# Kernel optimization log

Measured on AMD Instinct MI355X. Metric: run time of the kernel, lower is better.

## Reference

```python
import jax, jax.numpy as jnp
import numpy as np

B, P, CD, RD, H, NR, OD, T = 1024, 22, 256, 64, 512, 12, 2, 100
IN = OD + 2 + CD + RD  # 324: [pos(2), ball(2), context(256), role_embed(64)]


def setup_inputs() -> dict:
    key = jax.random.key(0)
    ks = jax.random.split(key, 20)
    def n(k, shape, s=1.0):
        return jax.random.normal(k, shape, dtype=jnp.float32) * s
    sH = 1.0 / np.sqrt(H)
    sI = 1.0 / np.sqrt(IN)
    return {
        "context": n(ks[0], (B, P, CD)),
        "initial_position": n(ks[1], (B, P, OD)),
        "ball_landing": n(ks[2], (B, 2)),
        "roles": jax.random.randint(ks[3], (B, P), 0, NR, dtype=jnp.int32),
        "max_steps": T,
        "role_table": n(ks[4], (NR, RD), 0.02),
        # LSTM layer 0 (input_dim=IN)
        "W_ih0": n(ks[5], (4 * H, IN), sI),
        "W_hh0": n(ks[6], (4 * H, H), sH),
        "b0": n(ks[7], (4 * H,), sH),  # b_ih + b_hh fused
        # LSTM layer 1 (input_dim=H)
        "W_ih1": n(ks[8], (4 * H, H), sH),
        "W_hh1": n(ks[9], (4 * H, H), sH),
        "b1": n(ks[10], (4 * H,), sH),
        # output MLP: H -> H//2 -> OD
        "W_fc1": n(ks[11], (H // 2, H), sH),
        "b_fc1": n(ks[12], (H // 2,), sH),
        "W_fc2": n(ks[13], (OD, H // 2), 1.0 / np.sqrt(H // 2)),
        "b_fc2": n(ks[14], (OD,), 0.02),
        # initial_pos_encoder: Linear(OD, H)
        "W_init": n(ks[15], (H, OD), 1.0 / np.sqrt(OD)),
        "b_init": n(ks[16], (H,), 0.02),
    }


def _lstm_cell(x, h, c, W_ih, W_hh, b):
    # PyTorch gate order: i, f, g, o
    gates = x @ W_ih.T + h @ W_hh.T + b  # [N, 4H]
    i, f, g, o = jnp.split(gates, 4, axis=-1)
    c_new = jax.nn.sigmoid(f) * c + jax.nn.sigmoid(i) * jnp.tanh(g)
    h_new = jax.nn.sigmoid(o) * jnp.tanh(c_new)
    return h_new, c_new


def reference(context, initial_position, ball_landing, roles, max_steps,
              role_table, W_ih0, W_hh0, b0, W_ih1, W_hh1, b1,
              W_fc1, b_fc1, W_fc2, b_fc2, W_init, b_init):
    batch, num_players, context_dim = context.shape
    N = batch * num_players
    out_dim = initial_position.shape[-1]

    ctx_flat = context.reshape(N, context_dim)
    role_flat = role_table[roles].reshape(N, -1)
    ball_flat = jnp.broadcast_to(ball_landing[:, None, :], (batch, num_players, 2)).reshape(N, 2)
    static = jnp.concatenate([ball_flat, ctx_flat, role_flat], axis=1)  # [N, IN-2]

    pos0 = initial_position.reshape(N, out_dim)
    h0 = pos0 @ W_init.T + b_init  # initial_pos_encoder into layer-0 hidden
    c0 = jnp.zeros_like(h0)
    h1 = jnp.zeros_like(h0)
    c1 = jnp.zeros_like(h0)

    def step(carry, _):
        pos, h0, c0, h1, c1 = carry
        x = jnp.concatenate([pos, static], axis=1)  # [N, IN]
        h0, c0 = _lstm_cell(x, h0, c0, W_ih0, W_hh0, b0)
        h1, c1 = _lstm_cell(h0, h1, c1, W_ih1, W_hh1, b1)
        # output MLP (dropout inactive in eval)
        nxt = jax.nn.relu(h1 @ W_fc1.T + b_fc1) @ W_fc2.T + b_fc2  # [N, OD]
        return (nxt, h0, c0, h1, c1), nxt

    _, preds = jax.lax.scan(step, (pos0, h0, c0, h1, c1), None, length=max_steps)
    # preds: [T, N, OD] -> [batch, num_players, T, OD]
    preds = preds.transpose(1, 0, 2).reshape(batch, num_players, max_steps, out_dim)
    return preds
```

## Files before the change

### kernel.cpp

```cpp
#include <hip/hip_runtime.h>
#include <cstdint>


#define DEVI __device__ __forceinline__

typedef __bf16 bf16x8 __attribute__((ext_vector_type(8)));
typedef float  f32x4  __attribute__((ext_vector_type(4)));
typedef float  f32x2  __attribute__((ext_vector_type(2)));
typedef unsigned short u16x4 __attribute__((ext_vector_type(4)));
typedef unsigned short u16x8 __attribute__((ext_vector_type(8)));

static constexpr int NROWS = 22528;
static constexpr int NROWSP = 22536;
static constexpr int T_STEPS = 100;
static constexpr int NBM = 176;

DEVI unsigned short f2bf(float f) {
  unsigned u = __float_as_uint(f);
  u = u + 0x7FFFu + ((u >> 16) & 1u);
  return (unsigned short)(u >> 16);
}
DEVI float bf2f(unsigned short h) { return __uint_as_float(((unsigned)h) << 16); }

DEVI float fast_sigmoid(float x) {
  float e = __builtin_amdgcn_exp2f(-1.442695041f * x);
  return __builtin_amdgcn_rcpf(1.0f + e);
}
DEVI float fast_tanh(float x) {
  float e = __builtin_amdgcn_exp2f(2.885390082f * x);
  return 1.0f - 2.0f * __builtin_amdgcn_rcpf(e + 1.0f);
}

DEVI void async_copy16(const void* g, void* l) {
  __builtin_amdgcn_global_load_lds(
      (const __attribute__((address_space(1))) void*)g,
      (__attribute__((address_space(3))) void*)l, 16, 0, 0);
}

#define GBAR   asm volatile("s_barrier" ::: "memory")

template <int KITERS, int KSWITCH>
DEVI void gemm_core(const unsigned short* __restrict__ A1, int lda1,
                    const unsigned short* __restrict__ A2, int lda2,
                    const unsigned short* __restrict__ B1, int ldb1,
                    const unsigned short* __restrict__ B2, int ldb2,
                    unsigned short* lds, f32x4 acc[4][4], int tid) {
  const int lane = tid & 63, wid = tid >> 6;
  const int wm = wid & 1, wn = wid >> 1;
  const int c16 = lane & 15, q = lane >> 4;
#pragma unroll
  for (int i = 0; i < 4; ++i)
#pragma unroll
    for (int j = 0; j < 4; ++j) acc[i][j] = f32x4{0.f, 0.f, 0.f, 0.f};
#pragma unroll
  for (int kt = 0; kt < KITERS; ++kt) {
    const bool sec = (kt >= KSWITCH);
    const unsigned short* Ab = sec ? A2 : A1;
    const unsigned short* Bb = sec ? B2 : B1;
    const int lda = sec ? lda2 : lda1;
    const int ldb = sec ? ldb2 : ldb1;
    const int kk = (sec ? (kt - KSWITCH) : kt) * 64;
    __syncthreads();
#pragma unroll
    for (int rd = 0; rd < 4; ++rd) {
      int p = rd * 256 + tid;
      int row = p >> 3, u = p & 7, ch = u ^ (row & 7);
      async_copy16(Ab + row * lda + kk + ch * 8, lds + p * 8);
      async_copy16(Bb + row * ldb + kk + ch * 8, lds + 8192 + p * 8);
    }
    __syncthreads();
#pragma unroll
    for (int s = 0; s < 2; ++s) {
      bf16x8 a[4], b[4];
#pragma unroll
      for (int mf = 0; mf < 4; ++mf) {
        int row = wm * 64 + mf * 16 + c16;
        int slot = row * 8 + ((s * 4 + q) ^ (row & 7));
        a[mf] = *(const bf16x8*)(lds + slot * 8);
      }
#pragma unroll
      for (int nf = 0; nf < 4; ++nf) {
        int row = wn * 64 + nf * 16 + c16;
        int slot = row * 8 + ((s * 4 + q) ^ (row & 7));
        b[nf] = *(const bf16x8*)(lds + 8192 + slot * 8);
      }
#pragma unroll
      for (int mf = 0; mf < 4; ++mf)
#pragma unroll
        for (int nf = 0; nf < 4; ++nf)
          acc[mf][nf] = __builtin_amdgcn_mfma_f32_16x16x32_bf16(a[mf], b[nf], acc[mf][nf], 0, 0, 0);
    }
  }
}

DEVI int orig_row(int j) {
  int tile = j >> 7, rem = j & 127;
  int half = rem >> 6, g = (rem >> 4) & 3, cc = rem & 15;
  return g * 512 + (tile * 32 + half * 16 + cc);
}

__global__ void k_prep_w(const float* __restrict__ Whh0, const float* __restrict__ Wih1,
                         const float* __restrict__ Whh1, const float* __restrict__ Wih0,
                         const float* __restrict__ Wfc1, const float* __restrict__ b0,
                         const float* __restrict__ b1,
                         unsigned short* __restrict__ W0p, unsigned short* __restrict__ Wc1p,
                         unsigned short* __restrict__ Wsp, unsigned short* __restrict__ Wfc1b,
                         float* __restrict__ Wposx, float* __restrict__ Wposy,
                         float* __restrict__ b0p4, float* __restrict__ b1p4) {
  int j = blockIdx.x;
  int k = threadIdx.x;
  int o = orig_row(j);
  W0p[j * 512 + k]         = f2bf(Whh0[o * 512 + k]);
  Wc1p[j * 1024 + k]       = f2bf(Wih1[o * 512 + k]);
  Wc1p[j * 1024 + 512 + k] = f2bf(Whh1[o * 512 + k]);
  if (k < 384) Wsp[j * 384 + k] = (k < 322) ? f2bf(Wih0[o * 324 + 2 + k]) : (unsigned short)0;
  if (k == 0) {
    int g = (j >> 4) & 3;
    int cg = (j >> 7) * 32 + ((j >> 6) & 1) * 16 + (j & 15);
    Wposx[cg * 4 + g] = Wih0[o * 324 + 0];
    Wposy[cg * 4 + g] = Wih0[o * 324 + 1];
    b0p4[cg * 4 + g] = b0[o];
    b1p4[cg * 4 + g] = b1[o];
  }
  if (j < 256) Wfc1b[j * 512 + k] = f2bf(Wfc1[j * 512 + k]);
}

__global__ void k_init_xs(const float* __restrict__ ball, const float* __restrict__ ctx,
                          const int* __restrict__ roles, const float* __restrict__ role_table,
                          unsigned short* __restrict__ Xs) {
  int n = blockIdx.x, col = threadIdx.x;
  int b = n / 22;
  float v;
  if (col < 2)        v = ball[b * 2 + col];
  else if (col < 258) v = ctx[(size_t)n * 256 + col - 2];
  else if (col < 322) v = role_table[roles[n] * 64 + col - 258];
  else                v = 0.f;
  Xs[(size_t)n * 384 + col] = f2bf(v);
}

__global__ void k_init_p(const float* __restrict__ pos0, const float* __restrict__ Winit,
                         const float* __restrict__ binit,
                         unsigned short* __restrict__ h0A, unsigned short* __restrict__ h1A,
                         float* __restrict__ c0, float* __restrict__ c1,
                         float* __restrict__ posb, unsigned short* __restrict__ SP2) {
  int idx = blockIdx.x * 256 + threadIdx.x;
  if (idx >= NROWSP * 512) return;
  int n = idx >> 9, c = idx & 511;
  if (n < NROWS) {
    float px = pos0[n * 2 + 0], py = pos0[n * 2 + 1];
    h0A[(size_t)n * 512 + c] = f2bf(binit[c] + Winit[c * 2 + 0] * px + Winit[c * 2 + 1] * py);
    if (c < 2) posb[n * 2 + c] = pos0[n * 2 + c];
  } else {
    h0A[(size_t)n * 512 + c] = 0;
    if (c < 2) posb[n * 2 + c] = 0.f;
    ((unsigned long long*)SP2)[(size_t)n * 512 + c] = 0ull;
  }
  h1A[(size_t)n * 512 + c] = 0;
  c0[idx] = 0.f;
  c1[idx] = 0.f;
}

__global__ void k_init_state(const float* __restrict__ pos0, const float* __restrict__ Winit,
                             const float* __restrict__ binit, unsigned short* __restrict__ Hcat,
                             float* __restrict__ c0, float* __restrict__ c1,
                             float* __restrict__ posb) {
  int idx = blockIdx.x * 256 + threadIdx.x;
  if (idx >= NROWS * 512) return;
  int n = idx >> 9, c = idx & 511;
  float px = pos0[n * 2 + 0], py = pos0[n * 2 + 1];
  float h0 = binit[c] + Winit[c * 2 + 0] * px + Winit[c * 2 + 1] * py;
  Hcat[(size_t)n * 1024 + c] = f2bf(h0);
  Hcat[(size_t)n * 1024 + 512 + c] = 0;
  c0[idx] = 0.f;
  c1[idx] = 0.f;
  if (c < 2) posb[n * 2 + c] = pos0[n * 2 + c];
}

__global__ __launch_bounds__(256) void k_static(const unsigned short* __restrict__ Xs,
                                                const unsigned short* __restrict__ Wsp,
                                                const float* __restrict__ b0p4,
                                                unsigned short* __restrict__ SP2) {
  __shared__ __align__(16) unsigned short lds[16384];
  int tid = threadIdx.x, bn = blockIdx.x, bm = blockIdx.y;
  f32x4 acc[4][4];
  const unsigned short* Ab = Xs + (size_t)bm * 128 * 384;
  const unsigned short* Bb = Wsp + (size_t)bn * 128 * 384;
  gemm_core<6, 6>(Ab, 384, Ab, 384, Bb, 384, Bb, 384, lds, acc, tid);
  int lane = tid & 63, wid = tid >> 6, wm = wid & 1, wn = wid >> 1;
  int c16 = lane & 15, q = lane >> 4;
  int cg = bn * 32 + wn * 16 + c16;
  f32x4 bb = *(const f32x4*)&b0p4[cg * 4];
#pragma unroll
  for (int mf = 0; mf < 4; ++mf) {
    int row0 = bm * 128 + wm * 64 + mf * 16 + q * 4;
#pragma unroll
    for (int r = 0; r < 4; ++r) {
      u16x4 v;
      v.x = f2bf(acc[mf][0][r] + bb.x);
      v.y = f2bf(acc[mf][1][r] + bb.y);
      v.z = f2bf(acc[mf][2][r] + bb.z);
      v.w = f2bf(acc[mf][3][r] + bb.w);
      ((u16x4*)SP2)[(size_t)(row0 + r) * 512 + cg] = v;
    }
  }
}


DEVI void stageA_p(const unsigned short* As, int rowbase, int coff,
                   unsigned short* dst, int tid) {
#pragma unroll
  for (int rd = 0; rd < 3; ++rd) {
    int p = rd * 512 + tid;
    int row = p >> 4, gp = p & 15;
    async_copy16(As + (size_t)(rowbase + row) * 512 + coff + (gp ^ (row & 7)) * 8,
                 dst + p * 8);
  }
}

DEVI void stageB_p(const char* Bnt, int ldb, int koff, unsigned short* dst, int tid) {
#pragma unroll
  for (int ks = 0; ks < 2; ++ks)
#pragma unroll
    for (int rd = 0; rd < 2; ++rd) {
      int p = rd * 512 + tid;
      int j = p >> 2, u = p & 3, ch = u ^ ((j >> 1) & 3);
      async_copy16(Bnt + (size_t)j * ldb + koff + ks * 64 + ch * 16,
                   dst + ks * 8192 + p * 8);
    }
}

template <int KT, int KSW>
DEVI void gemm_p(const unsigned short* A1, const unsigned short* A2, int rowbase,
                 const char* Bnt, int ldb,
                 unsigned short* Abuf, unsigned short* Bbuf,
                 f32x4 acc[3][4], int tid) {
  const int lane = tid & 63, wid = tid >> 6;
  const int wm = wid >> 2, wn = wid & 3;
  const int c16 = lane & 15, q = lane >> 4;
#pragma unroll
  for (int i = 0; i < 3; ++i)
#pragma unroll
    for (int j = 0; j < 4; ++j) acc[i][j] = f32x4{0.f, 0.f, 0.f, 0.f};
  stageA_p(A1, rowbase, 0, Abuf, tid);
  stageB_p(Bnt, ldb, 0, Bbuf, tid);
#pragma unroll
  for (int kt = 0; kt < KT; ++kt) {
    GBAR;
    int nIss = 0;
    if (kt + 1 < KT) { stageB_p(Bnt, ldb, (kt + 1) * 128, Bbuf + ((kt + 1) & 1) * 16384, tid); nIss += 4; }
    if ((kt & 1) == 0 && (kt / 2 + 1) < KT / 2) {
      int c = kt / 2 + 1;
      const unsigned short* As = (c < KSW / 2) ? A1 : A2;
      int coff = ((c < KSW / 2) ? c : (c - KSW / 2)) * 128;
      stageA_p(As, rowbase, coff, Abuf + (c & 1) * 12288, tid);
      nIss += 3;
    }
    if (nIss == 7)      asm volatile("s_waitcnt vmcnt(7)" ::: "memory");
    else if (nIss == 4) asm volatile("s_waitcnt vmcnt(4)" ::: "memory");
    else if (nIss == 3) asm volatile("s_waitcnt vmcnt(3)" ::: "memory");
    else                asm volatile("s_waitcnt vmcnt(0)" ::: "memory");
    GBAR;
    const unsigned short* Ab = Abuf + ((kt >> 1) & 1) * 12288;
    const unsigned short* Bb = Bbuf + (kt & 1) * 16384;
#pragma unroll
    for (int ks = 0; ks < 2; ++ks) {
      bf16x8 a[3], b[4];
#pragma unroll
      for (int mf = 0; mf < 3; ++mf) {
        int rl = wm * 48 + mf * 16 + c16;
        int g = (kt & 1) * 8 + ks * 4 + q;
        a[mf] = *(const bf16x8*)(Ab + rl * 128 + (g ^ (rl & 7)) * 8);
      }
#pragma unroll
      for (int nf = 0; nf < 4; ++nf) {
        int jl = wn * 64 + nf * 16 + c16;
        b[nf] = *(const bf16x8*)(Bb + ks * 8192 + (jl * 4 + (q ^ ((jl >> 1) & 3))) * 8);
      }
      __builtin_amdgcn_s_setprio(1);
#pragma unroll
      for (int mf = 0; mf < 3; ++mf)
#pragma unroll
        for (int nf = 0; nf < 4; ++nf)
          acc[mf][nf] = __builtin_amdgcn_mfma_f32_16x16x32_bf16(a[mf], b[nf], acc[mf][nf], 0, 0, 0);
      __builtin_amdgcn_s_setprio(0);
    }
    __builtin_amdgcn_sched_barrier(0);
  }
}

__global__ __launch_bounds__(512, 2) void k_persist(
    const unsigned short* __restrict__ W0p, const unsigned short* __restrict__ Wc1p,
    const unsigned short* __restrict__ Wfc1b, const unsigned short* __restrict__ SP2,
    const float* __restrict__ b1p4,
    const float* __restrict__ Wposx, const float* __restrict__ Wposy,
    const float* __restrict__ bfc1, const float* __restrict__ Wfc2,
    const float* __restrict__ bfc2,
    unsigned short* __restrict__ h0A, unsigned short* __restrict__ h0B,
    unsigned short* __restrict__ h1A, unsigned short* __restrict__ h1B,
    float* __restrict__ c0, float* __restrict__ c1,
    float* __restrict__ posb, float* __restrict__ out) {
  __shared__ __align__(16) unsigned short Abuf[2 * 12288];
  __shared__ __align__(16) unsigned short Bbuf[2 * 16384];
  __shared__ float wfc2s[512];
  __shared__ float red[96 * 8];
  const int tid = threadIdx.x, blk = blockIdx.x;
  const int lane = tid & 63, wid = tid >> 6;
  const int wm = wid >> 2, wn = wid & 3;
  const int c16 = lane & 15, q = lane >> 4;
  const int rowbase = blk * 88;
  wfc2s[tid] = Wfc2[tid];
  __syncthreads();
  f32x4 acc[3][4];
#pragma unroll 1
  for (int t = 0; t < T_STEPS; ++t) {
    const unsigned short* h0p = (t & 1) ? h0B : h0A;
    unsigned short*       h0n = (t & 1) ? h0A : h0B;
    const unsigned short* h1p = (t & 1) ? h1B : h1A;
    unsigned short*       h1n = (t & 1) ? h1A : h1B;
#pragma unroll 1
    for (int nt = 0; nt < 8; ++nt) {
      gemm_p<8, 8>(h0p, h0p, rowbase, (const char*)W0p + (size_t)nt * 256 * 1024, 1024,
                   Abuf, Bbuf, acc, tid);
      const int cg = nt * 64 + (wn >> 1) * 32 + (wn & 1) * 16 + c16;
      f32x4 wpx = *(const f32x4*)&Wposx[cg * 4];
      f32x4 wpy = *(const f32x4*)&Wposy[cg * 4];
#pragma unroll
      for (int mf = 0; mf < 3; ++mf) {
        int row0 = rowbase + wm * 48 + mf * 16 + q * 4;
        f32x4 cold = *(const f32x4*)&c0[(size_t)cg * NROWSP + row0];
        f32x4 cnew;
#pragma unroll
        for (int r = 0; r < 4; ++r) {
          size_t row = row0 + r;
          f32x2 pv = *(const f32x2*)&posb[row * 2];
          u16x4 sp = ((const u16x4*)SP2)[row * 512 + cg];
          float gi = acc[mf][0][r] + bf2f(sp.x) + pv.x * wpx.x + pv.y * wpy.x;
          float gf = acc[mf][1][r] + bf2f(sp.y) + pv.x * wpx.y + pv.y * wpy.y;
          float gg = acc[mf][2][r] + bf2f(sp.z) + pv.x * wpx.z + pv.y * wpy.z;
          float go = acc[mf][3][r] + bf2f(sp.w) + pv.x * wpx.w + pv.y * wpy.w;
          float cn = fast_sigmoid(gf) * cold[r] + fast_sigmoid(gi) * fast_tanh(gg);
          cnew[r] = cn;
          h0n[row * 512 + cg] = f2bf(fast_sigmoid(go) * fast_tanh(cn));
        }
        *(f32x4*)&c0[(size_t)cg * NROWSP + row0] = cnew;
      }
      __syncthreads();
    }
#pragma unroll 1
    for (int nt = 0; nt < 8; ++nt) {
      gemm_p<16, 8>(h0n, h1p, rowbase, (const char*)Wc1p + (size_t)nt * 256 * 2048, 2048,
                    Abuf, Bbuf, acc, tid);
      const int cg = nt * 64 + (wn >> 1) * 32 + (wn & 1) * 16 + c16;
      f32x4 bv = *(const f32x4*)&b1p4[cg * 4];
#pragma unroll
      for (int mf = 0; mf < 3; ++mf) {
        int row0 = rowbase + wm * 48 + mf * 16 + q * 4;
        f32x4 cold = *(const f32x4*)&c1[(size_t)cg * NROWSP + row0];
        f32x4 cnew;
#pragma unroll
        for (int r = 0; r < 4; ++r) {
          size_t row = row0 + r;
          float gi = acc[mf][0][r] + bv.x;
          float gf = acc[mf][1][r] + bv.y;
          float gg = acc[mf][2][r] + bv.z;
          float go = acc[mf][3][r] + bv.w;
          float cn = fast_sigmoid(gf) * cold[r] + fast_sigmoid(gi) * fast_tanh(gg);
          cnew[r] = cn;
          h1n[row * 512 + cg] = f2bf(fast_sigmoid(go) * fast_tanh(cn));
        }
        *(f32x4*)&c1[(size_t)cg * NROWSP + row0] = cnew;
      }
      __syncthreads();
    }
    {
      gemm_p<8, 8>(h1n, h1n, rowbase, (const char*)Wfc1b, 1024, Abuf, Bbuf, acc, tid);
      float part[2][3][4];
#pragma unroll
      for (int d = 0; d < 2; ++d)
#pragma unroll
        for (int mf = 0; mf < 3; ++mf)
#pragma unroll
          for (int r = 0; r < 4; ++r) part[d][mf][r] = 0.f;
#pragma unroll
      for (int nf = 0; nf < 4; ++nf) {
        int col = wn * 64 + nf * 16 + c16;
        float w0 = wfc2s[col], w1 = wfc2s[256 + col], bv = bfc1[col];
#pragma unroll
        for (int mf = 0; mf < 3; ++mf)
#pragma unroll
          for (int r = 0; r < 4; ++r) {
            float v = acc[mf][nf][r] + bv;
            v = v > 0.f ? v : 0.f;
            part[0][mf][r] += v * w0;
            part[1][mf][r] += v * w1;
          }
      }
#pragma unroll
      for (int st = 1; st < 16; st <<= 1)
#pragma unroll
        for (int d = 0; d < 2; ++d)
#pragma unroll
          for (int mf = 0; mf < 3; ++mf)
#pragma unroll
            for (int r = 0; r < 4; ++r)
              part[d][mf][r] += __shfl_xor(part[d][mf][r], st, 64);
      if (c16 == 0) {
#pragma unroll
        for (int mf = 0; mf < 3; ++mf)
#pragma unroll
          for (int r = 0; r < 4; ++r) {
            int rl = wm * 48 + mf * 16 + q * 4 + r;
            red[rl * 8 + wn * 2 + 0] = part[0][mf][r];
            red[rl * 8 + wn * 2 + 1] = part[1][mf][r];
          }
      }
      __syncthreads();
      if (tid < 192) {
        int rl = tid >> 1, d = tid & 1;
        float s = red[rl * 8 + d] + red[rl * 8 + 2 + d] + red[rl * 8 + 4 + d]
                + red[rl * 8 + 6 + d] + bfc2[d];
        if (rl < 88) {
          int rg = rowbase + rl;
          out[((size_t)rg * T_STEPS + t) * 2 + d] = s;
          posb[rg * 2 + d] = s;
        }
      }
      __syncthreads();
    }
  }
}

struct GemmSrc {
  const unsigned short *A1, *A2, *B1, *B2;
  int ldA1, ldA2, ldB1, ldB2;
};

template <int KT, int KSW>
DEVI void stage_q(const GemmSrc& g, int t, int s, int isB, unsigned short* dst, int tid) {
  int tt = (t >= KT) ? (t - 2) : t;
  const bool sec = (tt >= KSW);
  const unsigned short* base;
  int ld;
  if (isB) { base = sec ? g.B2 : g.B1; ld = sec ? g.ldB2 : g.ldB1; }
  else     { base = sec ? g.A2 : g.A1; ld = sec ? g.ldA2 : g.ldA1; }
  base += (sec ? (tt - KSW) : tt) * 64 + s * 32;
#pragma unroll
  for (int rd = 0; rd < 2; ++rd) {
    int p = rd * 512 + tid;
    int row = p >> 2, u = p & 3, ch = u ^ ((row >> 1) & 3);
    async_copy16(base + row * ld + ch * 8, dst + p * 8);
  }
}

#define VMCNT4 asm volatile("s_waitcnt vmcnt(4)" ::: "memory")

template <int KT, int KSW>
DEVI void gemm8(const GemmSrc& g, unsigned short* lds, f32x4 acc[8][4], int tid) {
  const int lane = tid & 63, wid = tid >> 6;
  const int wm = wid >> 2, wn = wid & 3;
  const int c16 = lane & 15, q = lane >> 4;
#pragma unroll
  for (int i = 0; i < 8; ++i)
#pragma unroll
    for (int j = 0; j < 4; ++j) acc[i][j] = f32x4{0.f, 0.f, 0.f, 0.f};
  unsigned short* A00 = lds;
  unsigned short* A01 = lds + 8192;
  unsigned short* B00 = lds + 16384;
  unsigned short* B01 = lds + 24576;
  unsigned short* A10 = lds + 32768;
  unsigned short* A11 = lds + 40960;
  unsigned short* B10 = lds + 49152;
  unsigned short* B11 = lds + 57344;
  const int rowA0 = wm * 128 + c16;
  const int rowB0 = wn * 64 + c16;
  stage_q<KT, KSW>(g, 0, 0, 0, A00, tid);
  stage_q<KT, KSW>(g, 0, 0, 1, B00, tid);
  stage_q<KT, KSW>(g, 0, 1, 0, A01, tid);
// ... 15 lines not shown
    int row = rowB0 + f * 16;                                                  \
    b[f] = *(const bf16x8*)((BASE) + (row * 4 + (q ^ ((row >> 1) & 3))) * 8);  \
  }
#define MFG(MG)                                                                \
  __builtin_amdgcn_s_setprio(1);                                               \
  _Pragma("unroll")                                                            \
  for (int f = 0; f < 4; ++f)                                                  \
    _Pragma("unroll")                                                          \
    for (int nf = 0; nf < 4; ++nf)                                             \
      acc[(MG) * 4 + f][nf] = __builtin_amdgcn_mfma_f32_16x16x32_bf16(         \
          a[f], b[nf], acc[(MG) * 4 + f][nf], 0, 0, 0);                        \
  __builtin_amdgcn_s_setprio(0);                                               \
  __builtin_amdgcn_sched_barrier(0);
#pragma unroll 1
  for (int it = 0; it < KT / 2; ++it) {
    const int t0 = 2 * it;
    LOADA(A00, 0); LOADB(B00);
    stage_q<KT, KSW>(g, t0 + 1, 1, 0, A11, tid);
    GBAR; MFG(0); GBAR;
    LOADA(A00, 1);
    stage_q<KT, KSW>(g, t0 + 1, 1, 1, B11, tid);
    GBAR; MFG(1); GBAR;
    LOADA(A01, 0); LOADB(B01);
    stage_q<KT, KSW>(g, t0 + 2, 0, 0, A00, tid);
    GBAR; MFG(0); GBAR;
    LOADA(A01, 1);
    stage_q<KT, KSW>(g, t0 + 2, 0, 1, B00, tid);
    GBAR; MFG(1); VMCNT4; GBAR;
    LOADA(A10, 0); LOADB(B10);
    stage_q<KT, KSW>(g, t0 + 2, 1, 0, A01, tid);
    GBAR; MFG(0); GBAR;
    LOADA(A10, 1);
    stage_q<KT, KSW>(g, t0 + 2, 1, 1, B01, tid);
    GBAR; MFG(1); GBAR;
    LOADA(A11, 0); LOADB(B11);
    stage_q<KT, KSW>(g, t0 + 3, 0, 0, A10, tid);
    GBAR; MFG(0); GBAR;
    LOADA(A11, 1);
    stage_q<KT, KSW>(g, t0 + 3, 0, 1, B10, tid);
    GBAR; MFG(1); VMCNT4; GBAR;
  }
  asm volatile("s_waitcnt vmcnt(0)" ::: "memory");
#undef LOADA
#undef LOADB
#undef MFG
}

DEVI void swz704(int l, int& bn, int& bm) {
  int xcd = l & 7, ii = l >> 3;
  bn = ii & 7;
  bm = (ii >> 3) * 8 + xcd;
}

__global__ __launch_bounds__(512, 2) void k_s1_lite(const unsigned short* __restrict__ cur,
                                                    const unsigned short* __restrict__ Xs,
                                                    const unsigned short* __restrict__ W0p,
                                                    const unsigned short* __restrict__ Wsp,
                                                    const float* __restrict__ b0p4,
                                                    const float* __restrict__ Wposx,
                                                    const float* __restrict__ Wposy,
                                                    const float* __restrict__ posb,
                                                    float* __restrict__ c0,
                                                    unsigned short* __restrict__ nxt) {
  __shared__ __align__(16) unsigned short lds[65536];
  const int tid = threadIdx.x;
  int bn, bm;
  swz704(blockIdx.x, bn, bm);
  f32x4 acc[8][4];
  GemmSrc g;
  g.A1 = cur + (size_t)bm * 256 * 1024; g.ldA1 = 1024;
  g.B1 = W0p + (size_t)bn * 256 * 512;  g.ldB1 = 512;
  g.A2 = Xs + (size_t)bm * 256 * 384;   g.ldA2 = 384;
  g.B2 = Wsp + (size_t)bn * 256 * 384;  g.ldB2 = 384;
  gemm8<14, 8>(g, lds, acc, tid);
  const int lane = tid & 63, wid = tid >> 6;
  const int wm = wid >> 2, wn = wid & 3;
  const int c16 = lane & 15, q = lane >> 4;
  const int cg = bn * 64 + (wn >> 1) * 32 + (wn & 1) * 16 + c16;
  f32x4 wpx = *(const f32x4*)&Wposx[cg * 4];
  f32x4 wpy = *(const f32x4*)&Wposy[cg * 4];
  f32x4 sb = *(const f32x4*)&b0p4[cg * 4];
#pragma unroll
  for (int mf = 0; mf < 8; ++mf) {
    int row0 = bm * 256 + wm * 128 + mf * 16 + q * 4;
    f32x4 cold = *(const f32x4*)&c0[(size_t)cg * NROWS + row0];
    f32x4 cnew;
#pragma unroll
    for (int r = 0; r < 4; ++r) {
      size_t row = row0 + r;
      f32x2 pv = *(const f32x2*)&posb[row * 2];
      float gi = acc[mf][0][r] + sb.x + pv.x * wpx.x + pv.y * wpy.x;
      float gf = acc[mf][1][r] + sb.y + pv.x * wpx.y + pv.y * wpy.y;
      float gg = acc[mf][2][r] + sb.z + pv.x * wpx.z + pv.y * wpy.z;
      float go = acc[mf][3][r] + sb.w + pv.x * wpx.w + pv.y * wpy.w;
      float cn = fast_sigmoid(gf) * cold[r] + fast_sigmoid(gi) * fast_tanh(gg);
      cnew[r] = cn;
      nxt[row * 1024 + cg] = f2bf(fast_sigmoid(go) * fast_tanh(cn));
    }
    *(f32x4*)&c0[(size_t)cg * NROWS + row0] = cnew;
  }
}

__global__ __launch_bounds__(512, 2) void k_s2_8(const unsigned short* __restrict__ nxt_in,
                                                 const unsigned short* __restrict__ cur,
                                                 const unsigned short* __restrict__ Wc1p,
                                                 const float* __restrict__ b1p4,
// ... 131 lines not shown
#pragma unroll
    for (int mf = 0; mf < 2; ++mf)
#pragma unroll
      for (int r = 0; r < 4; ++r) {
        int rl = mf * 16 + q * 4 + r;
        red[rl * 8 + wid * 2 + 0] = part[0][mf][r];
        red[rl * 8 + wid * 2 + 1] = part[1][mf][r];
      }
  }
  __syncthreads();
  if (tid < 64) {
    int rl = tid >> 1, d = tid & 1;
    float s = red[rl * 8 + d] + red[rl * 8 + 2 + d] + red[rl * 8 + 4 + d]
            + red[rl * 8 + 6 + d] + bfc2[d];
    int rg = b32 * 32 + rl;
    out[((size_t)rg * T_STEPS + t) * 2 + d] = s;
    posb[rg * 2 + d] = s;
  }
}

extern "C" void kernel_launch(void* const* d_in, const int* in_sizes, int n_in,
                              void* d_out, int out_size, void* d_ws, size_t ws_size,
                              hipStream_t stream) {
  (void)in_sizes; (void)n_in; (void)out_size;
  const float* ctx   = (const float*)d_in[0];
  const float* pos0  = (const float*)d_in[1];
  const float* ball  = (const float*)d_in[2];
  const int*   roles = (const int*)d_in[3];
  const float* role_table = (const float*)d_in[5];
  const float* Wih0 = (const float*)d_in[6];
  const float* Whh0 = (const float*)d_in[7];
  const float* b0   = (const float*)d_in[8];
  const float* Wih1 = (const float*)d_in[9];
  const float* Whh1 = (const float*)d_in[10];
  const float* b1   = (const float*)d_in[11];
  const float* Wfc1 = (const float*)d_in[12];
  const float* bfc1 = (const float*)d_in[13];
  const float* Wfc2 = (const float*)d_in[14];
  const float* bfc2 = (const float*)d_in[15];
  const float* Winit = (const float*)d_in[16];
  const float* binit = (const float*)d_in[17];
  float* out = (float*)d_out;

  char* w = (char*)d_ws;
  size_t used = 0;
  auto alloc = [&](size_t bytes) {
    char* p = w + used;
    used += (bytes + 255) & ~(size_t)255;
    return p;
  };
  unsigned short* W0p   = (unsigned short*)alloc((size_t)2048 * 512 * 2);
  unsigned short* Wc1p  = (unsigned short*)alloc((size_t)2048 * 1024 * 2);
  unsigned short* Wfc1b = (unsigned short*)alloc((size_t)256 * 512 * 2);
  float* Wposx = (float*)alloc(2048 * 4);
  float* Wposy = (float*)alloc(2048 * 4);
  float* b0p4  = (float*)alloc(2048 * 4);
  float* b1p4  = (float*)alloc(2048 * 4);
  float* posb  = (float*)alloc((size_t)NROWSP * 2 * 4);
  unsigned short* h0A = (unsigned short*)alloc((size_t)NROWSP * 512 * 2);
  unsigned short* h0B = (unsigned short*)alloc((size_t)NROWSP * 512 * 2);
  unsigned short* h1A = (unsigned short*)alloc((size_t)NROWSP * 512 * 2);
  unsigned short* h1B = (unsigned short*)alloc((size_t)NROWSP * 512 * 2);
  float* c0   = (float*)alloc((size_t)512 * NROWSP * 4);
  float* c1   = (float*)alloc((size_t)512 * NROWSP * 4);
  unsigned short* SP2 = (unsigned short*)alloc((size_t)NROWSP * 2048 * 2);
  unsigned short* Xs  = h0B;
  unsigned short* Wsp = h1B;

  const bool use_p = (ws_size >= used + (1u << 20));

  if (use_p) {
    k_prep_w<<<2048, 512, 0, stream>>>(Whh0, Wih1, Whh1, Wih0, Wfc1, b0, b1,
                                       W0p, Wc1p, Wsp, Wfc1b, Wposx, Wposy, b0p4, b1p4);
    k_init_xs<<<NROWS, 384, 0, stream>>>(ball, ctx, roles, role_table, Xs);
    k_init_p<<<(NROWSP * 512 + 255) / 256, 256, 0, stream>>>(pos0, Winit, binit,
                                                             h0A, h1A, c0, c1, posb, SP2);
    dim3 gs(16, NBM);
    k_static<<<gs, 256, 0, stream>>>(Xs, Wsp, b0p4, SP2);
    k_persist<<<256, 512, 0, stream>>>(W0p, Wc1p, Wfc1b, SP2, b1p4, Wposx, Wposy,
                                       bfc1, Wfc2, bfc2, h0A, h0B, h1A, h1B,
                                       c0, c1, posb, out);
  } else {
    used = 0;
    unsigned short* W0pL   = (unsigned short*)alloc((size_t)2048 * 512 * 2);
    unsigned short* Wc1pL  = (unsigned short*)alloc((size_t)2048 * 1024 * 2);
    unsigned short* Wfc1bL = (unsigned short*)alloc((size_t)256 * 512 * 2);
    float* WposxL = (float*)alloc(2048 * 4);
    float* WposyL = (float*)alloc(2048 * 4);
    float* b0p4L  = (float*)alloc(2048 * 4);
    float* b1p4L  = (float*)alloc(2048 * 4);
    float* posbL  = (float*)alloc((size_t)NROWS * 2 * 4);
    unsigned short* Hc0 = (unsigned short*)alloc((size_t)NROWS * 1024 * 2);
    float* c0L   = (float*)alloc((size_t)NROWS * 512 * 4);
    float* c1L   = (float*)alloc((size_t)NROWS * 512 * 4);
    unsigned short* Hc1 = (unsigned short*)alloc((size_t)NROWS * 1024 * 2);
    unsigned short* XsL  = (unsigned short*)alloc((size_t)NROWS * 384 * 2);
    unsigned short* WspL = (unsigned short*)alloc((size_t)2048 * 384 * 2);

    k_prep_w<<<2048, 512, 0, stream>>>(Whh0, Wih1, Whh1, Wih0, Wfc1, b0, b1,
                                       W0pL, Wc1pL, WspL, Wfc1bL, WposxL, WposyL, b0p4L, b1p4L);
    k_init_xs<<<NROWS, 384, 0, stream>>>(ball, ctx, roles, role_table, XsL);
    k_init_state<<<(NROWS * 512 + 255) / 256, 256, 0, stream>>>(pos0, Winit, binit, Hc0,
                                                                c0L, c1L, posbL);
    for (int t = 0; t < T_STEPS; ++t) {
      unsigned short* cur = (t & 1) ? Hc1 : Hc0;
      unsigned short* nxt = (t & 1) ? Hc0 : Hc1;
      k_s1_lite<<<704, 512, 0, stream>>>(cur, XsL, W0pL, WspL, b0p4L,
                                         WposxL, WposyL, posbL, c0L, nxt);
      k_s2_8<<<704, 512, 0, stream>>>(nxt, cur, Wc1pL, b1p4L, c1L, nxt);
      k_s3<<<704, 256, 0, stream>>>(nxt, Wfc1bL, bfc1, Wfc2, bfc2, out, posbL, t);
    }
  }
}
```

Measured before the change: 21.52 ms.

## Fold static input projection into per-step layer-0 GEMM and halve persistent block size

Drops the precomputed static-gate buffer (SP2) and the separate static GEMM kernel. The layer-0 GEMM in the persistent kernel now concatenates h0 with the static inputs Xs along K (28 k-iters of 64 instead of 8 of 128), so the static projection is recomputed every timestep rather than read as a 22536x2048 bf16 buffer. The persistent kernel moves from 256 blocks of 512 threads with 88 rows each to 512 blocks of 256 threads with 44 rows each, with one M-wave per block. This trades a large per-step memory read for extra MFMA work each step and changes the occupancy and tiling, while removing the preprocessing GEMM.

```diff
diff --git a/kernel.cpp b/kernel.cpp
--- a/kernel.cpp
+++ b/kernel.cpp
@@ -8,12 +8,10 @@
 typedef float  f32x4  __attribute__((ext_vector_type(4)));
 typedef float  f32x2  __attribute__((ext_vector_type(2)));
 typedef unsigned short u16x4 __attribute__((ext_vector_type(4)));
-typedef unsigned short u16x8 __attribute__((ext_vector_type(8)));
 
 static constexpr int NROWS = 22528;
 static constexpr int NROWSP = 22536;
 static constexpr int T_STEPS = 100;
-static constexpr int NBM = 176;
 
 DEVI unsigned short f2bf(float f) {
   unsigned u = __float_as_uint(f);
@@ -37,61 +35,7 @@
       (__attribute__((address_space(3))) void*)l, 16, 0, 0);
 }
 
-#define GBAR   asm volatile("s_barrier" ::: "memory")
-
-template <int KITERS, int KSWITCH>
-DEVI void gemm_core(const unsigned short* __restrict__ A1, int lda1,
-                    const unsigned short* __restrict__ A2, int lda2,
-                    const unsigned short* __restrict__ B1, int ldb1,
-                    const unsigned short* __restrict__ B2, int ldb2,
-                    unsigned short* lds, f32x4 acc[4][4], int tid) {
-  const int lane = tid & 63, wid = tid >> 6;
-  const int wm = wid & 1, wn = wid >> 1;
-  const int c16 = lane & 15, q = lane >> 4;
-#pragma unroll
-  for (int i = 0; i < 4; ++i)
-#pragma unroll
-    for (int j = 0; j < 4; ++j) acc[i][j] = f32x4{0.f, 0.f, 0.f, 0.f};
-#pragma unroll
-  for (int kt = 0; kt < KITERS; ++kt) {
-    const bool sec = (kt >= KSWITCH);
-    const unsigned short* Ab = sec ? A2 : A1;
-    const unsigned short* Bb = sec ? B2 : B1;
-    const int lda = sec ? lda2 : lda1;
-    const int ldb = sec ? ldb2 : ldb1;
-    const int kk = (sec ? (kt - KSWITCH) : kt) * 64;
-    __syncthreads();
-#pragma unroll
-    for (int rd = 0; rd < 4; ++rd) {
-      int p = rd * 256 + tid;
-      int row = p >> 3, u = p & 7, ch = u ^ (row & 7);
-      async_copy16(Ab + row * lda + kk + ch * 8, lds + p * 8);
-      async_copy16(Bb + row * ldb + kk + ch * 8, lds + 8192 + p * 8);
-    }
-    __syncthreads();
-#pragma unroll
-    for (int s = 0; s < 2; ++s) {
-      bf16x8 a[4], b[4];
-#pragma unroll
-      for (int mf = 0; mf < 4; ++mf) {
-        int row = wm * 64 + mf * 16 + c16;
-        int slot = row * 8 + ((s * 4 + q) ^ (row & 7));
-        a[mf] = *(const bf16x8*)(lds + slot * 8);
-      }
-#pragma unroll
-      for (int nf = 0; nf < 4; ++nf) {
-        int row = wn * 64 + nf * 16 + c16;
-        int slot = row * 8 + ((s * 4 + q) ^ (row & 7));
-        b[nf] = *(const bf16x8*)(lds + 8192 + slot * 8);
-      }
-#pragma unroll
-      for (int mf = 0; mf < 4; ++mf)
-#pragma unroll
-        for (int nf = 0; nf < 4; ++nf)
-          acc[mf][nf] = __builtin_amdgcn_mfma_f32_16x16x32_bf16(a[mf], b[nf], acc[mf][nf], 0, 0, 0);
-    }
-  }
-}
+#define GBAR asm volatile("s_barrier" ::: "memory")
 
 DEVI int orig_row(int j) {
   int tile = j >> 7, rem = j & 127;
@@ -125,16 +69,17 @@
   if (j < 256) Wfc1b[j * 512 + k] = f2bf(Wfc1[j * 512 + k]);
 }
 
-__global__ void k_init_xs(const float* __restrict__ ball, const float* __restrict__ ctx,
-                          const int* __restrict__ roles, const float* __restrict__ role_table,
-                          unsigned short* __restrict__ Xs) {
+__global__ void k_init_xs_p(const float* __restrict__ ball, const float* __restrict__ ctx,
+                            const int* __restrict__ roles, const float* __restrict__ role_table,
+                            unsigned short* __restrict__ Xs) {
   int n = blockIdx.x, col = threadIdx.x;
-  int b = n / 22;
-  float v;
-  if (col < 2)        v = ball[b * 2 + col];
-  else if (col < 258) v = ctx[(size_t)n * 256 + col - 2];
-  else if (col < 322) v = role_table[roles[n] * 64 + col - 258];
-  else                v = 0.f;
+  float v = 0.f;
+  if (n < NROWS) {
+    int b = n / 22;
+    if (col < 2)        v = ball[b * 2 + col];
+    else if (col < 258) v = ctx[(size_t)n * 256 + col - 2];
+    else if (col < 322) v = role_table[roles[n] * 64 + col - 258];
+  }
   Xs[(size_t)n * 384 + col] = f2bf(v);
 }
 
@@ -142,117 +87,79 @@
                          const float* __restrict__ binit,
                          unsigned short* __restrict__ h0A, unsigned short* __restrict__ h1A,
                          float* __restrict__ c0, float* __restrict__ c1,
-                         float* __restrict__ posb, unsigned short* __restrict__ SP2) {
+                         float* __restrict__ posb) {
   int idx = blockIdx.x * 256 + threadIdx.x;
   if (idx >= NROWSP * 512) return;
   int n = idx >> 9, c = idx & 511;
+  unsigned short h0 = 0;
   if (n < NROWS) {
     float px = pos0[n * 2 + 0], py = pos0[n * 2 + 1];
-    h0A[(size_t)n * 512 + c] = f2bf(binit[c] + Winit[c * 2 + 0] * px + Winit[c * 2 + 1] * py);
+    h0 = f2bf(binit[c] + Winit[c * 2 + 0] * px + Winit[c * 2 + 1] * py);
     if (c < 2) posb[n * 2 + c] = pos0[n * 2 + c];
   } else {
-    h0A[(size_t)n * 512 + c] = 0;
     if (c < 2) posb[n * 2 + c] = 0.f;
-    ((unsigned long long*)SP2)[(size_t)n * 512 + c] = 0ull;
-  }
+  }
+  h0A[(size_t)n * 512 + c] = h0;
   h1A[(size_t)n * 512 + c] = 0;
   c0[idx] = 0.f;
   c1[idx] = 0.f;
 }
 
-__global__ void k_init_state(const float* __restrict__ pos0, const float* __restrict__ Winit,
-                             const float* __restrict__ binit, unsigned short* __restrict__ Hcat,
-                             float* __restrict__ c0, float* __restrict__ c1,
-                             float* __restrict__ posb) {
-  int idx = blockIdx.x * 256 + threadIdx.x;
-  if (idx >= NROWS * 512) return;
-  int n = idx >> 9, c = idx & 511;
-  float px = pos0[n * 2 + 0], py = pos0[n * 2 + 1];
-  float h0 = binit[c] + Winit[c * 2 + 0] * px + Winit[c * 2 + 1] * py;
-  Hcat[(size_t)n * 1024 + c] = f2bf(h0);
-  Hcat[(size_t)n * 1024 + 512 + c] = 0;
-  c0[idx] = 0.f;
-  c1[idx] = 0.f;
-  if (c < 2) posb[n * 2 + c] = pos0[n * 2 + c];
-}
-
-__global__ __launch_bounds__(256) void k_static(const unsigned short* __restrict__ Xs,
-                                                const unsigned short* __restrict__ Wsp,
-                                                const float* __restrict__ b0p4,
-                                                unsigned short* __restrict__ SP2) {
-  __shared__ __align__(16) unsigned short lds[16384];
-  int tid = threadIdx.x, bn = blockIdx.x, bm = blockIdx.y;
-  f32x4 acc[4][4];
-  const unsigned short* Ab = Xs + (size_t)bm * 128 * 384;
-  const unsigned short* Bb = Wsp + (size_t)bn * 128 * 384;
-  gemm_core<6, 6>(Ab, 384, Ab, 384, Bb, 384, Bb, 384, lds, acc, tid);
-  int lane = tid & 63, wid = tid >> 6, wm = wid & 1, wn = wid >> 1;
-  int c16 = lane & 15, q = lane >> 4;
-  int cg = bn * 32 + wn * 16 + c16;
-  f32x4 bb = *(const f32x4*)&b0p4[cg * 4];
-#pragma unroll
-  for (int mf = 0; mf < 4; ++mf) {
-    int row0 = bm * 128 + wm * 64 + mf * 16 + q * 4;
-#pragma unroll
-    for (int r = 0; r < 4; ++r) {
-      u16x4 v;
-      v.x = f2bf(acc[mf][0][r] + bb.x);
-      v.y = f2bf(acc[mf][1][r] + bb.y);
-      v.z = f2bf(acc[mf][2][r] + bb.z);
-      v.w = f2bf(acc[mf][3][r] + bb.w);
-      ((u16x4*)SP2)[(size_t)(row0 + r) * 512 + cg] = v;
-    }
-  }
-}
-
-
-DEVI void stageA_p(const unsigned short* As, int rowbase, int coff,
-                   unsigned short* dst, int tid) {
+
+DEVI void stA2(const unsigned short* As, int lda, int rb, int coff,
+               unsigned short* dst, int tid) {
 #pragma unroll
   for (int rd = 0; rd < 3; ++rd) {
-    int p = rd * 512 + tid;
+    int p = rd * 256 + tid;
     int row = p >> 4, gp = p & 15;
-    async_copy16(As + (size_t)(rowbase + row) * 512 + coff + (gp ^ (row & 7)) * 8,
+    async_copy16(As + (size_t)(rb + row) * lda + coff + (gp ^ (row & 7)) * 8,
                  dst + p * 8);
   }
 }
 
-DEVI void stageB_p(const char* Bnt, int ldb, int koff, unsigned short* dst, int tid) {
-#pragma unroll
-  for (int ks = 0; ks < 2; ++ks)
-#pragma unroll
-    for (int rd = 0; rd < 2; ++rd) {
-      int p = rd * 512 + tid;
-      int j = p >> 2, u = p & 3, ch = u ^ ((j >> 1) & 3);
-      async_copy16(Bnt + (size_t)j * ldb + koff + ks * 64 + ch * 16,
-                   dst + ks * 8192 + p * 8);
-    }
-}
-
-template <int KT, int KSW>
-DEVI void gemm_p(const unsigned short* A1, const unsigned short* A2, int rowbase,
-                 const char* Bnt, int ldb,
-                 unsigned short* Abuf, unsigned short* Bbuf,
-                 f32x4 acc[3][4], int tid) {
-  const int lane = tid & 63, wid = tid >> 6;
-  const int wm = wid >> 2, wn = wid & 3;
+DEVI void stB2(const char* B, int ldb, int koff, unsigned short* dst, int tid) {
+#pragma unroll
+  for (int rd = 0; rd < 4; ++rd) {
+    int p = rd * 256 + tid;
+    int j = p >> 2, u = p & 3, ch = u ^ ((j >> 1) & 3);
+    async_copy16(B + (size_t)j * ldb + koff + ch * 16, dst + p * 8);
+  }
+}
+
+struct Src2 {
+  const unsigned short *A1, *A2; int ldA1, ldA2;
+  const char *B1, *B2; int ldB1, ldB2;
+};
+
+template <int KT, int ASW, int BSW>
+DEVI void gemm2(const Src2& s, int rb, unsigned short* Ab2, unsigned short* Bb2,
+                f32x4 acc[3][4], int tid) {
+  const int lane = tid & 63, wn = tid >> 6;
   const int c16 = lane & 15, q = lane >> 4;
 #pragma unroll
   for (int i = 0; i < 3; ++i)
 #pragma unroll
     for (int j = 0; j < 4; ++j) acc[i][j] = f32x4{0.f, 0.f, 0.f, 0.f};
-  stageA_p(A1, rowbase, 0, Abuf, tid);
-  stageB_p(Bnt, ldb, 0, Bbuf, tid);
+  stA2(s.A1, s.ldA1, rb, 0, Ab2, tid);
+  stB2(s.B1, s.ldB1, 0, Bb2, tid);
 #pragma unroll
   for (int kt = 0; kt < KT; ++kt) {
     GBAR;
     int nIss = 0;
-    if (kt + 1 < KT) { stageB_p(Bnt, ldb, (kt + 1) * 128, Bbuf + ((kt + 1) & 1) * 16384, tid); nIss += 4; }
-    if ((kt & 1) == 0 && (kt / 2 + 1) < KT / 2) {
-      int c = kt / 2 + 1;
-      const unsigned short* As = (c < KSW / 2) ? A1 : A2;
-      int coff = ((c < KSW / 2) ? c : (c - KSW / 2)) * 128;
-      stageA_p(As, rowbase, coff, Abuf + (c & 1) * 12288, tid);
+    if (kt + 1 < KT) {
+      const int kb = kt + 1;
+      const char* Bp = (kb < BSW) ? s.B1 : s.B2;
+      const int ldb = (kb < BSW) ? s.ldB1 : s.ldB2;
+      const int ko = ((kb < BSW) ? kb : (kb - BSW)) * 64;
+      stB2(Bp, ldb, ko, Bb2 + (kb & 1) * 8192, tid);
+      nIss += 4;
+    }
+    if ((kt & 3) == 0 && (kt / 4 + 1) < KT / 4) {
+      const int c = kt / 4 + 1;
+      const unsigned short* Ap = (c < ASW) ? s.A1 : s.A2;
+      const int lda = (c < ASW) ? s.ldA1 : s.ldA2;
+      const int co = ((c < ASW) ? c : (c - ASW)) * 128;
+      stA2(Ap, lda, rb, co, Ab2 + (c & 1) * 6144, tid);
       nIss += 3;
     }
     if (nIss == 7)      asm volatile("s_waitcnt vmcnt(7)" ::: "memory");
@@ -260,38 +167,36 @@
     else if (nIss == 3) asm volatile("s_waitcnt vmcnt(3)" ::: "memory");
     else                asm volatile("s_waitcnt vmcnt(0)" ::: "memory");
     GBAR;
-    const unsigned short* Ab = Abuf + ((kt >> 1) & 1) * 12288;
-    const unsigned short* Bb = Bbuf + (kt & 1) * 16384;
-#pragma unroll
-    for (int ks = 0; ks < 2; ++ks) {
-      bf16x8 a[3], b[4];
-#pragma unroll
-      for (int mf = 0; mf < 3; ++mf) {
-        int rl = wm * 48 + mf * 16 + c16;
-        int g = (kt & 1) * 8 + ks * 4 + q;
-        a[mf] = *(const bf16x8*)(Ab + rl * 128 + (g ^ (rl & 7)) * 8);
-      }
-#pragma unroll
-      for (int nf = 0; nf < 4; ++nf) {
-        int jl = wn * 64 + nf * 16 + c16;
-        b[nf] = *(const bf16x8*)(Bb + ks * 8192 + (jl * 4 + (q ^ ((jl >> 1) & 3))) * 8);
-      }
-      __builtin_amdgcn_s_setprio(1);
-#pragma unroll
-      for (int mf = 0; mf < 3; ++mf)
-#pragma unroll
-        for (int nf = 0; nf < 4; ++nf)
-          acc[mf][nf] = __builtin_amdgcn_mfma_f32_16x16x32_bf16(a[mf], b[nf], acc[mf][nf], 0, 0, 0);
-      __builtin_amdgcn_s_setprio(0);
-    }
+    const unsigned short* Ab = Ab2 + ((kt >> 2) & 1) * 6144;
+    const unsigned short* Bb = Bb2 + (kt & 1) * 8192;
+    bf16x8 a[3], b[4];
+#pragma unroll
+    for (int mf = 0; mf < 3; ++mf) {
+      int rl = mf * 16 + c16;
+      int g = (kt & 3) * 4 + q;
+      a[mf] = *(const bf16x8*)(Ab + (rl * 16 + (g ^ (rl & 7))) * 8);
+    }
+#pragma unroll
+    for (int nf = 0; nf < 4; ++nf) {
+      int jl = wn * 64 + nf * 16 + c16;
+      b[nf] = *(const bf16x8*)(Bb + (jl * 4 + (q ^ ((jl >> 1) & 3))) * 8);
+    }
+    __builtin_amdgcn_s_setprio(1);
+#pragma unroll
+    for (int mf = 0; mf < 3; ++mf)
+#pragma unroll
+      for (int nf = 0; nf < 4; ++nf)
+        acc[mf][nf] = __builtin_amdgcn_mfma_f32_16x16x32_bf16(a[mf], b[nf], acc[mf][nf], 0, 0, 0);
+    __builtin_amdgcn_s_setprio(0);
     __builtin_amdgcn_sched_barrier(0);
   }
 }
 
-__global__ __launch_bounds__(512, 2) void k_persist(
+__global__ __launch_bounds__(256, 2) void k_persist2(
     const unsigned short* __restrict__ W0p, const unsigned short* __restrict__ Wc1p,
-    const unsigned short* __restrict__ Wfc1b, const unsigned short* __restrict__ SP2,
-    const float* __restrict__ b1p4,
+    const unsigned short* __restrict__ Wfc1b, const unsigned short* __restrict__ Wsp,
+    const unsigned short* __restrict__ Xs,
+    const float* __restrict__ b0p4, const float* __restrict__ b1p4,
     const float* __restrict__ Wposx, const float* __restrict__ Wposy,
     const float* __restrict__ bfc1, const float* __restrict__ Wfc2,
     const float* __restrict__ bfc2,
@@ -299,16 +204,16 @@
     unsigned short* __restrict__ h1A, unsigned short* __restrict__ h1B,
     float* __restrict__ c0, float* __restrict__ c1,
     float* __restrict__ posb, float* __restrict__ out) {
-  __shared__ __align__(16) unsigned short Abuf[2 * 12288];
-  __shared__ __align__(16) unsigned short Bbuf[2 * 16384];
+  __shared__ __align__(16) unsigned short Ab2[2 * 6144];
+  __shared__ __align__(16) unsigned short Bb2[2 * 8192];
   __shared__ float wfc2s[512];
-  __shared__ float red[96 * 8];
+  __shared__ float red[48 * 8];
   const int tid = threadIdx.x, blk = blockIdx.x;
-  const int lane = tid & 63, wid = tid >> 6;
-  const int wm = wid >> 2, wn = wid & 3;
+  const int lane = tid & 63, wn = tid >> 6;
   const int c16 = lane & 15, q = lane >> 4;
-  const int rowbase = blk * 88;
+  const int rb = blk * 44;
   wfc2s[tid] = Wfc2[tid];
+  wfc2s[tid + 256] = Wfc2[tid + 256];
   __syncthreads();
   f32x4 acc[3][4];
 #pragma unroll 1
@@ -319,42 +224,50 @@
     unsigned short*       h1n = (t & 1) ? h1A : h1B;
 #pragma unroll 1
     for (int nt = 0; nt < 8; ++nt) {
-      gemm_p<8, 8>(h0p, h0p, rowbase, (const char*)W0p + (size_t)nt * 256 * 1024, 1024,
-                   Abuf, Bbuf, acc, tid);
+      Src2 s;
+      s.A1 = h0p; s.ldA1 = 512; s.A2 = Xs; s.ldA2 = 384;
+      s.B1 = (const char*)W0p + (size_t)nt * 256 * 1024; s.ldB1 = 1024;
+      s.B2 = (const char*)Wsp + (size_t)nt * 256 * 768;  s.ldB2 = 768;
+      gemm2<28, 4, 16>(s, rb, Ab2, Bb2, acc, tid);
       const int cg = nt * 64 + (wn >> 1) * 32 + (wn & 1) * 16 + c16;
       f32x4 wpx = *(const f32x4*)&Wposx[cg * 4];
       f32x4 wpy = *(const f32x4*)&Wposy[cg * 4];
+      f32x4 sb  = *(const f32x4*)&b0p4[cg * 4];
 #pragma unroll
       for (int mf = 0; mf < 3; ++mf) {
-        int row0 = rowbase + wm * 48 + mf * 16 + q * 4;
+        const bool live = !(mf == 2 && q == 3);
+        int row0 = rb + mf * 16 + q * 4;
         f32x4 cold = *(const f32x4*)&c0[(size_t)cg * NROWSP + row0];
         f32x4 cnew;
 #pragma unroll
         for (int r = 0; r < 4; ++r) {
           size_t row = row0 + r;
           f32x2 pv = *(const f32x2*)&posb[row * 2];
-          u16x4 sp = ((const u16x4*)SP2)[row * 512 + cg];
-          float gi = acc[mf][0][r] + bf2f(sp.x) + pv.x * wpx.x + pv.y * wpy.x;
-          float gf = acc[mf][1][r] + bf2f(sp.y) + pv.x * wpx.y + pv.y * wpy.y;
-          float gg = acc[mf][2][r] + bf2f(sp.z) + pv.x * wpx.z + pv.y * wpy.z;
-          float go = acc[mf][3][r] + bf2f(sp.w) + pv.x * wpx.w + pv.y * wpy.w;
+          float gi = acc[mf][0][r] + sb.x + pv.x * wpx.x + pv.y * wpy.x;
+          float gf = acc[mf][1][r] + sb.y + pv.x * wpx.y + pv.y * wpy.y;
+          float gg = acc[mf][2][r] + sb.z + pv.x * wpx.z + pv.y * wpy.z;
+          float go = acc[mf][3][r] + sb.w + pv.x * wpx.w + pv.y * wpy.w;
           float cn = fast_sigmoid(gf) * cold[r] + fast_sigmoid(gi) * fast_tanh(gg);
           cnew[r] = cn;
-          h0n[row * 512 + cg] = f2bf(fast_sigmoid(go) * fast_tanh(cn));
+          if (live) h0n[row * 512 + cg] = f2bf(fast_sigmoid(go) * fast_tanh(cn));
         }
-        *(f32x4*)&c0[(size_t)cg * NROWSP + row0] = cnew;
+        if (live) *(f32x4*)&c0[(size_t)cg * NROWSP + row0] = cnew;
       }
       __syncthreads();
     }
 #pragma unroll 1
     for (int nt = 0; nt < 8; ++nt) {
-      gemm_p<16, 8>(h0n, h1p, rowbase, (const char*)Wc1p + (size_t)nt * 256 * 2048, 2048,
-                    Abuf, Bbuf, acc, tid);
+      Src2 s;
+      s.A1 = h0n; s.ldA1 = 512; s.A2 = h1p; s.ldA2 = 512;
+      s.B1 = (const char*)Wc1p + (size_t)nt * 256 * 2048; s.ldB1 = 2048;
+      s.B2 = s.B1; s.ldB2 = 2048;
+      gemm2<32, 4, 32>(s, rb, Ab2, Bb2, acc, tid);
       const int cg = nt * 64 + (wn >> 1) * 32 + (wn & 1) * 16 + c16;
       f32x4 bv = *(const f32x4*)&b1p4[cg * 4];
 #pragma unroll
       for (int mf = 0; mf < 3; ++mf) {
-        int row0 = rowbase + wm * 48 + mf * 16 + q * 4;
+        const bool live = !(mf == 2 && q == 3);
+        int row0 = rb + mf * 16 + q * 4;
         f32x4 cold = *(const f32x4*)&c1[(size_t)cg * NROWSP + row0];
         f32x4 cnew;
 #pragma unroll
@@ -366,14 +279,18 @@
           float go = acc[mf][3][r] + bv.w;
           float cn = fast_sigmoid(gf) * cold[r] + fast_sigmoid(gi) * fast_tanh(gg);
           cnew[r] = cn;
-          h1n[row * 512 + cg] = f2bf(fast_sigmoid(go) * fast_tanh(cn));
+          if (live) h1n[row * 512 + cg] = f2bf(fast_sigmoid(go) * fast_tanh(cn));
         }
-        *(f32x4*)&c1[(size_t)cg * NROWSP + row0] = cnew;
+        if (live) *(f32x4*)&c1[(size_t)cg * NROWSP + row0] = cnew;
       }
       __syncthreads();
     }
     {
-      gemm_p<8, 8>(h1n, h1n, rowbase, (const char*)Wfc1b, 1024, Abuf, Bbuf, acc, tid);
+      Src2 s;
+      s.A1 = h1n; s.ldA1 = 512; s.A2 = h1n; s.ldA2 = 512;
+      s.B1 = (const char*)Wfc1b; s.ldB1 = 1024;
+      s.B2 = s.B1; s.ldB2 = 1024;
+      gemm2<16, 4, 16>(s, rb, Ab2, Bb2, acc, tid);
       float part[2][3][4];
 #pragma unroll
       for (int d = 0; d < 2; ++d)
@@ -409,20 +326,20 @@
         for (int mf = 0; mf < 3; ++mf)
 #pragma unroll
           for (int r = 0; r < 4; ++r) {
-            int rl = wm * 48 + mf * 16 + q * 4 + r;
+            int rl = mf * 16 + q * 4 + r;
             red[rl * 8 + wn * 2 + 0] = part[0][mf][r];
             red[rl * 8 + wn * 2 + 1] = part[1][mf][r];
           }
       }
       __syncthreads();
-      if (tid < 192) {
+      if (tid < 96) {
         int rl = tid >> 1, d = tid & 1;
-        float s = red[rl * 8 + d] + red[rl * 8 + 2 + d] + red[rl * 8 + 4 + d]
-                + red[rl * 8 + 6 + d] + bfc2[d];
-        if (rl < 88) {
-          int rg = rowbase + rl;
-          out[((size_t)rg * T_STEPS + t) * 2 + d] = s;
-          posb[rg * 2 + d] = s;
+        float sum = red[rl * 8 + d] + red[rl * 8 + 2 + d] + red[rl * 8 + 4 + d]
+                  + red[rl * 8 + 6 + d] + bfc2[d];
+        if (rl < 44) {
+          int rg = rb + rl;
+          out[((size_t)rg * T_STEPS + t) * 2 + d] = sum;
+          posb[(size_t)rg * 2 + d] = sum;
         }
       }
       __syncthreads();
@@ -544,6 +461,35 @@
   bm = (ii >> 3) * 8 + xcd;
 }
 
+__global__ void k_init_xs(const float* __restrict__ ball, const float* __restrict__ ctx,
+                          const int* __restrict__ roles, const float* __restrict__ role_table,
+                          unsigned short* __restrict__ Xs) {
+  int n = blockIdx.x, col = threadIdx.x;
+  int b = n / 22;
+  float v;
+  if (col < 2)        v = ball[b * 2 + col];
+  else if (col < 258) v = ctx[(size_t)n * 256 + col - 2];
+  else if (col < 322) v = role_table[roles[n] * 64 + col - 258];
+  else                v = 0.f;
+  Xs[(size_t)n * 384 + col] = f2bf(v);
+}
+
+__global__ void k_init_state(const float* __restrict__ pos0, const float* __restrict__ Winit,
+                             const float* __restrict__ binit, unsigned short* __restrict__ Hcat,
+                             float* __restrict__ c0, float* __restrict__ c1,
+                             float* __restrict__ posb) {
+  int idx = blockIdx.x * 256 + threadIdx.x;
+  if (idx >= NROWS * 512) return;
+  int n = idx >> 9, c = idx & 511;
+  float px = pos0[n * 2 + 0], py = pos0[n * 2 + 1];
+  float h0 = binit[c] + Winit[c * 2 + 0] * px + Winit[c * 2 + 1] * py;
+  Hcat[(size_t)n * 1024 + c] = f2bf(h0);
+  Hcat[(size_t)n * 1024 + 512 + c] = 0;
+  c0[idx] = 0.f;
+  c1[idx] = 0.f;
+  if (c < 2) posb[n * 2 + c] = pos0[n * 2 + c];
+}
+
 __global__ __launch_bounds__(512, 2) void k_s1_lite(const unsigned short* __restrict__ cur,
                                                     const unsigned short* __restrict__ Xs,
                                                     const unsigned short* __restrict__ W0p,
@@ -781,34 +727,30 @@
   unsigned short* W0p   = (unsigned short*)alloc((size_t)2048 * 512 * 2);
   unsigned short* Wc1p  = (unsigned short*)alloc((size_t)2048 * 1024 * 2);
   unsigned short* Wfc1b = (unsigned short*)alloc((size_t)256 * 512 * 2);
+  unsigned short* Wsp   = (unsigned short*)alloc((size_t)2048 * 384 * 2);
   float* Wposx = (float*)alloc(2048 * 4);
   float* Wposy = (float*)alloc(2048 * 4);
   float* b0p4  = (float*)alloc(2048 * 4);
   float* b1p4  = (float*)alloc(2048 * 4);
   float* posb  = (float*)alloc((size_t)NROWSP * 2 * 4);
+  unsigned short* Xs  = (unsigned short*)alloc((size_t)NROWSP * 384 * 2);
   unsigned short* h0A = (unsigned short*)alloc((size_t)NROWSP * 512 * 2);
   unsigned short* h0B = (unsigned short*)alloc((size_t)NROWSP * 512 * 2);
   unsigned short* h1A = (unsigned short*)alloc((size_t)NROWSP * 512 * 2);
   unsigned short* h1B = (unsigned short*)alloc((size_t)NROWSP * 512 * 2);
-  float* c0   = (float*)alloc((size_t)512 * NROWSP * 4);
-  float* c1   = (float*)alloc((size_t)512 * NROWSP * 4);
-  unsigned short* SP2 = (unsigned short*)alloc((size_t)NROWSP * 2048 * 2);
-  unsigned short* Xs  = h0B;
-  unsigned short* Wsp = h1B;
-
-  const bool use_p = (ws_size >= used + (1u << 20));
+  float* c0 = (float*)alloc((size_t)512 * NROWSP * 4);
+  float* c1 = (float*)alloc((size_t)512 * NROWSP * 4);
+  const bool use_p = (ws_size >= used);
 
   if (use_p) {
     k_prep_w<<<2048, 512, 0, stream>>>(Whh0, Wih1, Whh1, Wih0, Wfc1, b0, b1,
                                        W0p, Wc1p, Wsp, Wfc1b, Wposx, Wposy, b0p4, b1p4);
-    k_init_xs<<<NROWS, 384, 0, stream>>>(ball, ctx, roles, role_table, Xs);
+    k_init_xs_p<<<NROWSP, 384, 0, stream>>>(ball, ctx, roles, role_table, Xs);
     k_init_p<<<(NROWSP * 512 + 255) / 256, 256, 0, stream>>>(pos0, Winit, binit,
-                                                             h0A, h1A, c0, c1, posb, SP2);
-    dim3 gs(16, NBM);
-    k_static<<<gs, 256, 0, stream>>>(Xs, Wsp, b0p4, SP2);
-    k_persist<<<256, 512, 0, stream>>>(W0p, Wc1p, Wfc1b, SP2, b1p4, Wposx, Wposy,
-                                       bfc1, Wfc2, bfc2, h0A, h0B, h1A, h1B,
-                                       c0, c1, posb, out);
+                                                             h0A, h1A, c0, c1, posb);
+    k_persist2<<<512, 256, 0, stream>>>(W0p, Wc1p, Wfc1b, Wsp, Xs, b0p4, b1p4,
+                                        Wposx, Wposy, bfc1, Wfc2, bfc2,
+                                        h0A, h0B, h1A, h1B, c0, c1, posb, out);
   } else {
     used = 0;
     unsigned short* W0pL   = (unsigned short*)alloc((size_t)2048 * 512 * 2);
@@ -827,7 +769,8 @@
     unsigned short* WspL = (unsigned short*)alloc((size_t)2048 * 384 * 2);
 
     k_prep_w<<<2048, 512, 0, stream>>>(Whh0, Wih1, Whh1, Wih0, Wfc1, b0, b1,
-                                       W0pL, Wc1pL, WspL, Wfc1bL, WposxL, WposyL, b0p4L, b1p4L);
+                                       W0pL, Wc1pL, WspL, Wfc1bL, WposxL, WposyL,
+                                       b0p4L, b1p4L);
     k_init_xs<<<NROWS, 384, 0, stream>>>(ball, ctx, roles, role_table, XsL);
     k_init_state<<<(NROWS * 512 + 255) / 256, 256, 0, stream>>>(pos0, Winit, binit, Hc0,
                                                                 c0L, c1L, posbL);
```

Result: slower. 42.24 ms (+96.2%).
